# Optimization experiments

Measured on AMD Instinct MI355X. Metric: run time of the kernel, lower is better.

## Reference

```python
import jax, jax.numpy as jnp
import numpy as np

N = 50000      # nodes
E = 800000     # edges (before self-loops)
G = 64         # graphs
F_IN = 128
HID = 64
HEADS = 2
OUT = 10
NEG_SLOPE = 0.2


def setup_inputs() -> dict:
    key = jax.random.key(0)
    ks = jax.random.split(key, 12)
    x = jax.random.normal(ks[0], (N, F_IN), dtype=jnp.float32)
    edge_index = jax.random.randint(ks[1], (2, E), 0, N, dtype=jnp.int64)
    batch = jnp.sort(jax.random.randint(ks[2], (N,), 0, G, dtype=jnp.int64))
    s = 0.1
    params = {
        "W1": jax.random.normal(ks[3], (F_IN, HEADS * HID), dtype=jnp.float32) * s,
        "att_src1": jax.random.normal(ks[4], (HEADS, HID), dtype=jnp.float32) * s,
        "att_dst1": jax.random.normal(ks[5], (HEADS, HID), dtype=jnp.float32) * s,
        "b1": jnp.zeros((HEADS * HID,), dtype=jnp.float32),
        "W2": jax.random.normal(ks[6], (HEADS * HID, HEADS * HID), dtype=jnp.float32) * s,
        "att_src2": jax.random.normal(ks[7], (HEADS, HID), dtype=jnp.float32) * s,
        "att_dst2": jax.random.normal(ks[8], (HEADS, HID), dtype=jnp.float32) * s,
        "b2": jnp.zeros((HEADS * HID,), dtype=jnp.float32),
        "Wl": jax.random.normal(ks[9], (HEADS * HID, OUT), dtype=jnp.float32) * s,
        "bl": jnp.zeros((OUT,), dtype=jnp.float32),
    }
    return {"x": x, "edge_index": edge_index, "batch": batch, **params}


def gat_conv(x, W, att_src, att_dst, bias, src, dst):
    # x: [N, Fin]; W: [Fin, H*C]
    h = (x @ W).reshape(N, HEADS, HID)                      # [N, H, C]
    a_src = jnp.sum(h * att_src, axis=-1)                   # [N, H]
    a_dst = jnp.sum(h * att_dst, axis=-1)                   # [N, H]
    alpha = jax.nn.leaky_relu(a_src[src] + a_dst[dst], NEG_SLOPE)  # [Etot, H]
    # segment softmax over incoming edges of each dst node
    m = jax.ops.segment_max(alpha, dst, num_segments=N)     # [N, H]
    alpha = jnp.exp(alpha - m[dst])
    denom = jax.ops.segment_sum(alpha, dst, num_segments=N)
    alpha = alpha / (denom[dst] + 1e-16)
    out = jax.ops.segment_sum(alpha[:, :, None] * h[src], dst, num_segments=N)
    return out.reshape(N, HEADS * HID) + bias


def reference(x, edge_index, batch, W1, att_src1, att_dst1, b1,
              W2, att_src2, att_dst2, b2, Wl, bl):
    # PyG GATConv default: add self-loops
    loop = jnp.arange(N, dtype=edge_index.dtype)
    src = jnp.concatenate([edge_index[0], loop])
    dst = jnp.concatenate([edge_index[1], loop])

    h = jax.nn.relu(gat_conv(x, W1, att_src1, att_dst1, b1, src, dst))
    h = jax.nn.relu(gat_conv(h, W2, att_src2, att_dst2, b2, src, dst))

    # global_mean_pool over graphs
    sums = jax.ops.segment_sum(h, batch, num_segments=G)        # [G, H*C]
    cnts = jax.ops.segment_sum(jnp.ones((N,), h.dtype), batch, num_segments=G)
    pooled = sums / jnp.maximum(cnts, 1.0)[:, None]
    return pooled @ Wl + bl                                      # [G, OUT]
```

## Files before the change

kernel.cpp:

```cpp
#include <hip/hip_runtime.h>
#include <hip/hip_fp16.h>
#include <math.h>

#define N_NODES 50000
#define N_EDGES 800000
#define ETOT    850000
#define GRAPHS  64
#define FIN     128
#define HC      128
#define OUTF    10
#define NEG     0.2f

#define NBUCK   196
#define BCAP    8192
#define EPT     8

using half8   = __attribute__((ext_vector_type(8))) _Float16;
using float4v = __attribute__((ext_vector_type(4))) float;

__global__ void initk(int* tails, float* sums) {
    int i = blockIdx.x * 256 + threadIdx.x;
    if (i < NBUCK) tails[i] = 0;
    if (i < GRAPHS * HC) sums[i] = 0.f;
}

__global__ void wconv(const float* __restrict__ W1, const float* __restrict__ W2,
                      _Float16* __restrict__ WT1, _Float16* __restrict__ WT2) {
    int t = blockIdx.x * 256 + threadIdx.x;
    if (t < 16384) {
        int n = t >> 7, k = t & 127;
        WT1[t] = (_Float16)W1[k * 128 + n];
        WT2[t] = (_Float16)W2[k * 128 + n];
    }
}

__global__ __launch_bounds__(256) void bucketA(const int* __restrict__ ei,
                                               int* __restrict__ tails,
                                               int* __restrict__ bdata) {
    __shared__ int hist[NBUCK];
    __shared__ int lbase[NBUCK];
    int t = threadIdx.x;
    int e0 = blockIdx.x * (256 * EPT);
    for (int i = t; i < NBUCK; i += 256) hist[i] = 0;
    __syncthreads();

    int bb[EPT], pk[EPT], rk[EPT];
#pragma unroll
    for (int i = 0; i < EPT; ++i) {
        int e = e0 + i * 256 + t;
        bb[i] = -1;
        if (e < ETOT) {
            int s, d;
            if (e < N_EDGES) { s = ei[e]; d = ei[N_EDGES + e]; }
            else             { s = d = e - N_EDGES; }
            bb[i] = d >> 8;
            pk[i] = s | ((d & 255) << 16);
            rk[i] = atomicAdd(&hist[bb[i]], 1);
        }
    }
    __syncthreads();
    for (int i = t; i < NBUCK; i += 256)
        lbase[i] = atomicAdd(&tails[i], hist[i]);
    __syncthreads();
#pragma unroll
    for (int i = 0; i < EPT; ++i)
        if (bb[i] >= 0) bdata[bb[i] * BCAP + lbase[bb[i]] + rk[i]] = pk[i];
}

__global__ void scanBuckets(const int* __restrict__ tails,
                            int* __restrict__ csrBase,
                            int* __restrict__ rowptr) {
    __shared__ int sh[256];
    int t = threadIdx.x;
    int c = (t < NBUCK) ? tails[t] : 0;
    sh[t] = c;
    __syncthreads();
    for (int off = 1; off < 256; off <<= 1) {
        int add = (t >= off) ? sh[t - off] : 0;
        __syncthreads();
        sh[t] += add;
        __syncthreads();
    }
    if (t < NBUCK) csrBase[t] = sh[t] - c;
    if (t == NBUCK - 1) rowptr[N_NODES] = sh[t];
}

__global__ __launch_bounds__(256) void bucketB(const int* __restrict__ bdata,
                                               const int* __restrict__ tails,
                                               const int* __restrict__ csrBase,
                                               int* __restrict__ rowptr,
                                               int* __restrict__ csr) {
    __shared__ int hist[256];
    __shared__ int scanws[256];
    int b = blockIdx.x;
    int t = threadIdx.x;
    int nodes0 = b << 8;
    int nnodes = min(256, N_NODES - nodes0);
    int cnt  = tails[b];
    int base = csrBase[b];
    const int* bd = &bdata[b * BCAP];

    hist[t] = 0;
    __syncthreads();
    for (int j = t; j < cnt; j += 256) atomicAdd(&hist[bd[j] >> 16], 1);
    __syncthreads();
    scanws[t] = hist[t];
    __syncthreads();
    for (int off = 1; off < 256; off <<= 1) {
        int add = (t >= off) ? scanws[t - off] : 0;
        __syncthreads();
        scanws[t] += add;
        __syncthreads();
    }
    int excl = scanws[t] - hist[t];
    if (t < nnodes) rowptr[nodes0 + t] = base + excl;
    __syncthreads();
    hist[t] = excl;
    __syncthreads();
    for (int j = t; j < cnt; j += 256) {
        int pkv = bd[j];
        int pos = atomicAdd(&hist[pkv >> 16], 1);
        csr[base + pos] = pkv & 0xFFFF;
    }
}

template<bool FP32IN>
__global__ __launch_bounds__(256) void gemmMFMA(const void* __restrict__ Xin,
                                                const _Float16* __restrict__ WT,
                                                const float* __restrict__ att_s,
                                                const float* __restrict__ att_d,
                                                _Float16* __restrict__ H16,
                                                float2* __restrict__ a_src,
                                                float2* __restrict__ a_dst) {
    __shared__ _Float16 wt[128][128];
    int t = threadIdx.x;

    for (int i = t; i < 128 * 16; i += 256) {
        int n = i >> 4, ch = i & 15;
        int k0 = ch * 8;
        half8 v = *(const half8*)&WT[n * 128 + k0];
        *(half8*)&wt[n][k0 ^ ((n & 7) << 3)] = v;
    }

    int w = t >> 6, lane = t & 63;
    int hi = lane >> 4, l16 = lane & 15;
    int rbase = blockIdx.x * 64 + w * 16;
    int arow = min(rbase + l16, N_NODES - 1);

    half8 a[4];
    if (FP32IN) {
        const float* X = (const float*)Xin;
#pragma unroll
        for (int kb = 0; kb < 4; ++kb) {
            int k0 = kb * 32 + hi * 8;
            float4 x0 = *(const float4*)&X[(size_t)arow * 128 + k0];
            float4 x1 = *(const float4*)&X[(size_t)arow * 128 + k0 + 4];
            half8 v;
            v[0] = (_Float16)x0.x; v[1] = (_Float16)x0.y;
            v[2] = (_Float16)x0.z; v[3] = (_Float16)x0.w;
            v[4] = (_Float16)x1.x; v[5] = (_Float16)x1.y;
            v[6] = (_Float16)x1.z; v[7] = (_Float16)x1.w;
            a[kb] = v;
        }
    } else {
        const _Float16* X = (const _Float16*)Xin;
#pragma unroll
        for (int kb = 0; kb < 4; ++kb)
            a[kb] = *(const half8*)&X[(size_t)arow * 128 + kb * 32 + hi * 8];
    }

    __syncthreads();

    float4v acc[8];
#pragma unroll
    for (int ct = 0; ct < 8; ++ct) {
        float4v c = {0.f, 0.f, 0.f, 0.f};
        int n = ct * 16 + l16;
#pragma unroll
        for (int kb = 0; kb < 4; ++kb) {
            int k0 = (kb * 32 + hi * 8) ^ ((n & 7) << 3);
            half8 b = *(const half8*)&wt[n][k0];
            c = __builtin_amdgcn_mfma_f32_16x16x32_f16(a[kb], b, c, 0, 0, 0);
        }
        acc[ct] = c;
    }

    int grow0 = rbase + hi * 4;
#pragma unroll
    for (int ct = 0; ct < 8; ++ct) {
#pragma unroll
        for (int r = 0; r < 4; ++r) {
            int grow = grow0 + r;
            if (grow < N_NODES)
                H16[(size_t)grow * 128 + ct * 16 + l16] = (_Float16)acc[ct][r];
        }
    }

    float as_[8], ad_[8];
#pragma unroll
    for (int ct = 0; ct < 8; ++ct) {
        as_[ct] = att_s[ct * 16 + l16];
        ad_[ct] = att_d[ct * 16 + l16];
    }
#pragma unroll
    for (int r = 0; r < 4; ++r) {
        float s0 = 0.f, s1 = 0.f, d0 = 0.f, d1 = 0.f;
#pragma unroll
        for (int ct = 0; ct < 4; ++ct) { s0 += acc[ct][r] * as_[ct]; d0 += acc[ct][r] * ad_[ct]; }
#pragma unroll
        for (int ct = 4; ct < 8; ++ct) { s1 += acc[ct][r] * as_[ct]; d1 += acc[ct][r] * ad_[ct]; }
        for (int off = 1; off < 16; off <<= 1) {
            s0 += __shfl_xor(s0, off); s1 += __shfl_xor(s1, off);
            d0 += __shfl_xor(d0, off); d1 += __shfl_xor(d1, off);
        }
        int grow = grow0 + r;
        if (l16 == 0 && grow < N_NODES) {
            a_src[grow] = make_float2(s0, s1);
            a_dst[grow] = make_float2(d0, d1);
        }
    }
}

__device__ __forceinline__ float leaky(float x) { return x > 0.f ? x : NEG * x; }

__global__ __launch_bounds__(256) void aggk(const __half* __restrict__ H16,
                                            const float2* __restrict__ a_src,
                                            const float2* __restrict__ a_dst,
                                            const int* __restrict__ rowptr,
                                            const int* __restrict__ csr,
                                            const float* __restrict__ bias,
                                            _Float16* __restrict__ out16) {
    int wid = (blockIdx.x * 256 + threadIdx.x) >> 6;
    int lane = threadIdx.x & 63;
    if (wid >= N_NODES) return;
    int rbeg = rowptr[wid], rend = rowptr[wid + 1];
    float2 ad = a_dst[wid];

    int grp = lane >> 3;
    int gl  = lane & 7;
    int head = gl >> 2;
    float adh = head ? ad.y : ad.x;
    int f = gl * 16;

    float acc[16];
#pragma unroll
    for (int i = 0; i < 16; ++i) acc[i] = 0.f;
    float denom = 0.f;

    int j = rbeg + grp;
    int sNext = (j < rend) ? csr[j] : 0;
    for (; j < rend; j += 8) {
        int s = sNext;
        int jn = j + 8;
        if (jn < rend) sNext = csr[jn];
        float2 as = a_src[s];
        float wgt = __expf(leaky((head ? as.y : as.x) + adh));
        const uint4* hp = (const uint4*)&H16[(size_t)s * 128 + f];
        uint4 r0 = hp[0];
        uint4 r1 = hp[1];
        float2 p;
        p = __half22float2(*(__half2*)&r0.x); acc[0] += wgt * p.x; acc[1] += wgt * p.y;
        p = __half22float2(*(__half2*)&r0.y); acc[2] += wgt * p.x; acc[3] += wgt * p.y;
        p = __half22float2(*(__half2*)&r0.z); acc[4] += wgt * p.x; acc[5] += wgt * p.y;
        p = __half22float2(*(__half2*)&r0.w); acc[6] += wgt * p.x; acc[7] += wgt * p.y;
        p = __half22float2(*(__half2*)&r1.x); acc[8] += wgt * p.x; acc[9] += wgt * p.y;
        p = __half22float2(*(__half2*)&r1.y); acc[10] += wgt * p.x; acc[11] += wgt * p.y;
        p = __half22float2(*(__half2*)&r1.z); acc[12] += wgt * p.x; acc[13] += wgt * p.y;
        p = __half22float2(*(__half2*)&r1.w); acc[14] += wgt * p.x; acc[15] += wgt * p.y;
        denom += wgt;
    }
#pragma unroll
    for (int off = 8; off <= 32; off <<= 1) {
#pragma unroll
        for (int i = 0; i < 16; ++i) acc[i] += __shfl_xor(acc[i], off);
        denom += __shfl_xor(denom, off);
    }

    if (grp == 0) {
        float inv = 1.f / (denom + 1e-16f);
        half8 h0, h1;
#pragma unroll
        for (int i = 0; i < 8; ++i) {
            float o = fmaxf(acc[i] * inv + bias[f + i], 0.f);
            h0[i] = (_Float16)o;
        }
#pragma unroll
        for (int i = 0; i < 8; ++i) {
            float o = fmaxf(acc[8 + i] * inv + bias[f + 8 + i], 0.f);
            h1[i] = (_Float16)o;
        }
        *(half8*)&out16[(size_t)wid * 128 + f]     = h0;
        *(half8*)&out16[(size_t)wid * 128 + f + 8] = h1;
    }
}

__global__ void countk(const int* __restrict__ batch, int* cnt) {
    int g = threadIdx.x;
    if (g >= GRAPHS) return;
    int lo = 0, hi = N_NODES;
    while (lo < hi) { int mid = (lo + hi) >> 1; if (batch[mid] < g) lo = mid + 1; else hi = mid; }
    int lb = lo;
    lo = 0; hi = N_NODES;
    while (lo < hi) { int mid = (lo + hi) >> 1; if (batch[mid] < g + 1) lo = mid + 1; else hi = mid; }
    cnt[g] = lo - lb;
}

__global__ void poolk(const _Float16* __restrict__ H, const int* __restrict__ batch,
                      float* __restrict__ sums) {
    int f = threadIdx.x;
    int n0 = blockIdx.x * 64;
    if (n0 >= N_NODES) return;
    int n1 = min(n0 + 64, N_NODES);
    int g = batch[n0];
    float run = 0.f;
    for (int n = n0; n < n1; ++n) {
        int gn = batch[n];
        if (gn != g) { atomicAdd(&sums[g * 128 + f], run); run = 0.f; g = gn; }
        run += (float)H[(size_t)n * 128 + f];
    }
    atomicAdd(&sums[g * 128 + f], run);
}

__global__ void finalk(const float* __restrict__ sums, const int* __restrict__ cnt,
                       const float* __restrict__ Wl, const float* __restrict__ bl,
                       float* __restrict__ out) {
    int t = threadIdx.x;
    if (t >= GRAPHS * OUTF) return;
    int g = t / OUTF, o = t % OUTF;
    float inv = 1.f / fmaxf((float)cnt[g], 1.f);
    float acc = 0.f;
#pragma unroll 8
    for (int k = 0; k < 128; ++k) acc += sums[g * 128 + k] * Wl[k * OUTF + o];
    out[t] = acc * inv + bl[o];
}

extern "C" void kernel_launch(void* const* d_in, const int* in_sizes, int n_in,
                              void* d_out, int out_size, void* d_ws, size_t ws_size,
                              hipStream_t stream) {
    const float* x        = (const float*)d_in[0];
    const int*   ei       = (const int*)d_in[1];
    const int*   batch    = (const int*)d_in[2];
    const float* W1       = (const float*)d_in[3];
    const float* att_src1 = (const float*)d_in[4];
    const float* att_dst1 = (const float*)d_in[5];
    const float* b1       = (const float*)d_in[6];
    const float* W2       = (const float*)d_in[7];
    const float* att_src2 = (const float*)d_in[8];
    const float* att_dst2 = (const float*)d_in[9];
    const float* b2       = (const float*)d_in[10];
    const float* Wl       = (const float*)d_in[11];
    const float* bl       = (const float*)d_in[12];
    float* out = (float*)d_out;

    size_t off = 0;
    auto alloc = [&](size_t bytes) -> void* {
        void* p = (char*)d_ws + off;
        off = (off + bytes + 255) & ~(size_t)255;
        return p;
    };
    _Float16* H16     = (_Float16*)alloc((size_t)N_NODES * 128 * 2);
    _Float16* B16     = (_Float16*)alloc((size_t)N_NODES * 128 * 2);
    _Float16* WT1     = (_Float16*)alloc(16384 * 2);
    _Float16* WT2     = (_Float16*)alloc(16384 * 2);
    float2*   a_src   = (float2*)alloc((size_t)N_NODES * 8);
    float2*   a_dst   = (float2*)alloc((size_t)N_NODES * 8);
    int*      bdata   = (int*)alloc((size_t)NBUCK * BCAP * 4);
    int*      tails   = (int*)alloc(NBUCK * 4);
    int*      csrBase = (int*)alloc(NBUCK * 4);
    int*      rowptr  = (int*)alloc((size_t)(N_NODES + 1) * 4);
    int*      csr     = (int*)alloc((size_t)ETOT * 4);
    float*    sums    = (float*)alloc((size_t)GRAPHS * HC * 4);
    int*      cnt     = (int*)alloc(GRAPHS * 4);

    initk<<<32, 256, 0, stream>>>(tails, sums);
    wconv<<<64, 256, 0, stream>>>(W1, W2, WT1, WT2);
    bucketA<<<(ETOT + 2047) / 2048, 256, 0, stream>>>(ei, tails, bdata);
    scanBuckets<<<1, 256, 0, stream>>>(tails, csrBase, rowptr);
    bucketB<<<NBUCK, 256, 0, stream>>>(bdata, tails, csrBase, rowptr, csr);

    const int gemmBlocks = (N_NODES + 63) / 64;
    const int waveBlocks = (N_NODES * 64 + 255) / 256;

    gemmMFMA<true><<<gemmBlocks, 256, 0, stream>>>(x, WT1, att_src1, att_dst1,
                                                   H16, a_src, a_dst);
    aggk<<<waveBlocks, 256, 0, stream>>>((const __half*)H16, a_src, a_dst,
                                         rowptr, csr, b1, B16);

    gemmMFMA<false><<<gemmBlocks, 256, 0, stream>>>(B16, WT2, att_src2, att_dst2,
                                                    H16, a_src, a_dst);
    aggk<<<waveBlocks, 256, 0, stream>>>((const __half*)H16, a_src, a_dst,
                                         rowptr, csr, b2, B16);

    countk<<<1, 64, 0, stream>>>(batch, cnt);
    poolk<<<(N_NODES + 63) / 64, 128, 0, stream>>>(B16, batch, sums);
    finalk<<<1, 640, 0, stream>>>(sums, cnt, Wl, bl, out);
}
```

Baseline: 173.7 us.

## Merge small kernels and co-schedule layer-1 GEMM with edge bucketing

Merges init and weight conversion into one setup kernel. It fuses the layer-1 GEMM and edge bucketing into one launch, with blocks split by index. It folds the bucket scan into each bucketB block and the graph-count binary search into finalk. The aggregation loop now prefetches a_src for the next edge alongside the next CSR index. The aim is to cut the launch count (from 11 to 7) and overlap independent work, in exchange for redundant scans per block and more LDS in the fused kernel.

```diff
diff --git a/kernel.cpp b/kernel.cpp
--- a/kernel.cpp
+++ b/kernel.cpp
@@ -14,33 +14,126 @@
 #define NBUCK   196
 #define BCAP    8192
 #define EPT     8
+#define GEMMB   782
+#define ABLK    416
 
 using half8   = __attribute__((ext_vector_type(8))) _Float16;
 using float4v = __attribute__((ext_vector_type(4))) float;
 
-__global__ void initk(int* tails, float* sums) {
+__global__ void setupk(const float* __restrict__ W1, const float* __restrict__ W2,
+                       _Float16* __restrict__ WT1, _Float16* __restrict__ WT2,
+                       int* __restrict__ tails, float* __restrict__ sums) {
     int i = blockIdx.x * 256 + threadIdx.x;
+    if (i < 16384) {
+        int n = i >> 7, k = i & 127;
+        WT1[i] = (_Float16)W1[k * 128 + n];
+        WT2[i] = (_Float16)W2[k * 128 + n];
+    }
     if (i < NBUCK) tails[i] = 0;
     if (i < GRAPHS * HC) sums[i] = 0.f;
 }
 
-__global__ void wconv(const float* __restrict__ W1, const float* __restrict__ W2,
-                      _Float16* __restrict__ WT1, _Float16* __restrict__ WT2) {
-    int t = blockIdx.x * 256 + threadIdx.x;
-    if (t < 16384) {
-        int n = t >> 7, k = t & 127;
-        WT1[t] = (_Float16)W1[k * 128 + n];
-        WT2[t] = (_Float16)W2[k * 128 + n];
-    }
-}
-
-__global__ __launch_bounds__(256) void bucketA(const int* __restrict__ ei,
-                                               int* __restrict__ tails,
-                                               int* __restrict__ bdata) {
-    __shared__ int hist[NBUCK];
-    __shared__ int lbase[NBUCK];
-    int t = threadIdx.x;
-    int e0 = blockIdx.x * (256 * EPT);
+template<bool FP32IN>
+__device__ __forceinline__ void gemm_body(int bid, int t, _Float16 (*wt)[128],
+                                          const void* __restrict__ Xin,
+                                          const _Float16* __restrict__ WT,
+                                          const float* __restrict__ att_s,
+                                          const float* __restrict__ att_d,
+                                          _Float16* __restrict__ H16,
+                                          float2* __restrict__ a_src,
+                                          float2* __restrict__ a_dst) {
+    for (int i = t; i < 128 * 16; i += 256) {
+        int n = i >> 4, ch = i & 15;
+        int k0 = ch * 8;
+        half8 v = *(const half8*)&WT[n * 128 + k0];
+        *(half8*)&wt[n][k0 ^ ((n & 7) << 3)] = v;
+    }
+
+    int w = t >> 6, lane = t & 63;
+    int hi = lane >> 4, l16 = lane & 15;
+    int rbase = bid * 64 + w * 16;
+    int arow = min(rbase + l16, N_NODES - 1);
+
+    half8 a[4];
+    if (FP32IN) {
+        const float* X = (const float*)Xin;
+#pragma unroll
+        for (int kb = 0; kb < 4; ++kb) {
+            int k0 = kb * 32 + hi * 8;
+            float4 x0 = *(const float4*)&X[(size_t)arow * 128 + k0];
+            float4 x1 = *(const float4*)&X[(size_t)arow * 128 + k0 + 4];
+            half8 v;
+            v[0] = (_Float16)x0.x; v[1] = (_Float16)x0.y;
+            v[2] = (_Float16)x0.z; v[3] = (_Float16)x0.w;
+            v[4] = (_Float16)x1.x; v[5] = (_Float16)x1.y;
+            v[6] = (_Float16)x1.z; v[7] = (_Float16)x1.w;
+            a[kb] = v;
+        }
+    } else {
+        const _Float16* X = (const _Float16*)Xin;
+#pragma unroll
+        for (int kb = 0; kb < 4; ++kb)
+            a[kb] = *(const half8*)&X[(size_t)arow * 128 + kb * 32 + hi * 8];
+    }
+
+    __syncthreads();
+
+    float4v acc[8];
+#pragma unroll
+    for (int ct = 0; ct < 8; ++ct) {
+        float4v c = {0.f, 0.f, 0.f, 0.f};
+        int n = ct * 16 + l16;
+#pragma unroll
+        for (int kb = 0; kb < 4; ++kb) {
+            int k0 = (kb * 32 + hi * 8) ^ ((n & 7) << 3);
+            half8 b = *(const half8*)&wt[n][k0];
+            c = __builtin_amdgcn_mfma_f32_16x16x32_f16(a[kb], b, c, 0, 0, 0);
+        }
+        acc[ct] = c;
+    }
+
+    int grow0 = rbase + hi * 4;
+#pragma unroll
+    for (int ct = 0; ct < 8; ++ct) {
+#pragma unroll
+        for (int r = 0; r < 4; ++r) {
+            int grow = grow0 + r;
+            if (grow < N_NODES)
+                H16[(size_t)grow * 128 + ct * 16 + l16] = (_Float16)acc[ct][r];
+        }
+    }
+
+    float as_[8], ad_[8];
+#pragma unroll
+    for (int ct = 0; ct < 8; ++ct) {
+        as_[ct] = att_s[ct * 16 + l16];
+        ad_[ct] = att_d[ct * 16 + l16];
+    }
+#pragma unroll
+    for (int r = 0; r < 4; ++r) {
+        float s0 = 0.f, s1 = 0.f, d0 = 0.f, d1 = 0.f;
+#pragma unroll
+        for (int ct = 0; ct < 4; ++ct) { s0 += acc[ct][r] * as_[ct]; d0 += acc[ct][r] * ad_[ct]; }
+#pragma unroll
+        for (int ct = 4; ct < 8; ++ct) { s1 += acc[ct][r] * as_[ct]; d1 += acc[ct][r] * ad_[ct]; }
+        for (int off = 1; off < 16; off <<= 1) {
+            s0 += __shfl_xor(s0, off); s1 += __shfl_xor(s1, off);
+            d0 += __shfl_xor(d0, off); d1 += __shfl_xor(d1, off);
+        }
+        int grow = grow0 + r;
+        if (l16 == 0 && grow < N_NODES) {
+            a_src[grow] = make_float2(s0, s1);
+            a_dst[grow] = make_float2(d0, d1);
+        }
+    }
+}
+
+__device__ __forceinline__ void bucketA_body(int bid, int t,
+                                             int* hist, int* lbase,
+                                             const int* __restrict__ ei,
+                                             int* __restrict__ tails,
+                                             int* __restrict__ bdata) {
+    int e0 = bid * (256 * EPT);
     for (int i = t; i < NBUCK; i += 256) hist[i] = 0;
     __syncthreads();
 
@@ -67,65 +160,28 @@
         if (bb[i] >= 0) bdata[bb[i] * BCAP + lbase[bb[i]] + rk[i]] = pk[i];
 }
 
-__global__ void scanBuckets(const int* __restrict__ tails,
-                            int* __restrict__ csrBase,
-                            int* __restrict__ rowptr) {
-    __shared__ int sh[256];
+__global__ __launch_bounds__(256) void fusedA(const float* __restrict__ x,
+                                              const _Float16* __restrict__ WT1,
+                                              const float* __restrict__ att_s,
+                                              const float* __restrict__ att_d,
+                                              _Float16* __restrict__ H16,
+                                              float2* __restrict__ a_src,
+                                              float2* __restrict__ a_dst,
+                                              const int* __restrict__ ei,
+                                              int* __restrict__ tails,
+                                              int* __restrict__ bdata) {
+    __shared__ _Float16 wt[128][128];
+    __shared__ int hist[NBUCK];
+    __shared__ int lbase[NBUCK];
     int t = threadIdx.x;
-    int c = (t < NBUCK) ? tails[t] : 0;
-    sh[t] = c;
-    __syncthreads();
-    for (int off = 1; off < 256; off <<= 1) {
-        int add = (t >= off) ? sh[t - off] : 0;
-        __syncthreads();
-        sh[t] += add;
-        __syncthreads();
-    }
-    if (t < NBUCK) csrBase[t] = sh[t] - c;
-    if (t == NBUCK - 1) rowptr[N_NODES] = sh[t];
-}
-
-__global__ __launch_bounds__(256) void bucketB(const int* __restrict__ bdata,
-                                               const int* __restrict__ tails,
-                                               const int* __restrict__ csrBase,
-                                               int* __restrict__ rowptr,
-                                               int* __restrict__ csr) {
-    __shared__ int hist[256];
-    __shared__ int scanws[256];
-    int b = blockIdx.x;
-    int t = threadIdx.x;
-    int nodes0 = b << 8;
-    int nnodes = min(256, N_NODES - nodes0);
-    int cnt  = tails[b];
-    int base = csrBase[b];
-    const int* bd = &bdata[b * BCAP];
-
-    hist[t] = 0;
-    __syncthreads();
-    for (int j = t; j < cnt; j += 256) atomicAdd(&hist[bd[j] >> 16], 1);
-    __syncthreads();
-    scanws[t] = hist[t];
-    __syncthreads();
-    for (int off = 1; off < 256; off <<= 1) {
-        int add = (t >= off) ? scanws[t - off] : 0;
-        __syncthreads();
-        scanws[t] += add;
-        __syncthreads();
-    }
-    int excl = scanws[t] - hist[t];
-    if (t < nnodes) rowptr[nodes0 + t] = base + excl;
-    __syncthreads();
-    hist[t] = excl;
-    __syncthreads();
-    for (int j = t; j < cnt; j += 256) {
-        int pkv = bd[j];
-        int pos = atomicAdd(&hist[pkv >> 16], 1);
-        csr[base + pos] = pkv & 0xFFFF;
-    }
-}
-
-template<bool FP32IN>
-__global__ __launch_bounds__(256) void gemmMFMA(const void* __restrict__ Xin,
+    if (blockIdx.x < GEMMB) {
+        gemm_body<true>(blockIdx.x, t, wt, x, WT1, att_s, att_d, H16, a_src, a_dst);
+    } else {
+        bucketA_body(blockIdx.x - GEMMB, t, hist, lbase, ei, tails, bdata);
+    }
+}
+
+__global__ __launch_bounds__(256) void gemmMFMA(const _Float16* __restrict__ Xin,
                                                 const _Float16* __restrict__ WT,
                                                 const float* __restrict__ att_s,
                                                 const float* __restrict__ att_d,
@@ -133,91 +189,56 @@
                                                 float2* __restrict__ a_src,
                                                 float2* __restrict__ a_dst) {
     __shared__ _Float16 wt[128][128];
+    gemm_body<false>(blockIdx.x, threadIdx.x, wt, Xin, WT, att_s, att_d, H16, a_src, a_dst);
+}
+
+__global__ __launch_bounds__(256) void bucketB(const int* __restrict__ bdata,
+                                               const int* __restrict__ tails,
+                                               int* __restrict__ rowptr,
+                                               int* __restrict__ csr) {
+    __shared__ int hist[256];
+    __shared__ int scanws[256];
+    int b = blockIdx.x;
     int t = threadIdx.x;
 
-    for (int i = t; i < 128 * 16; i += 256) {
-        int n = i >> 4, ch = i & 15;
-        int k0 = ch * 8;
-        half8 v = *(const half8*)&WT[n * 128 + k0];
-        *(half8*)&wt[n][k0 ^ ((n & 7) << 3)] = v;
-    }
-
-    int w = t >> 6, lane = t & 63;
-    int hi = lane >> 4, l16 = lane & 15;
-    int rbase = blockIdx.x * 64 + w * 16;
-    int arow = min(rbase + l16, N_NODES - 1);
-
-    half8 a[4];
-    if (FP32IN) {
-        const float* X = (const float*)Xin;
-#pragma unroll
-        for (int kb = 0; kb < 4; ++kb) {
-            int k0 = kb * 32 + hi * 8;
-            float4 x0 = *(const float4*)&X[(size_t)arow * 128 + k0];
-            float4 x1 = *(const float4*)&X[(size_t)arow * 128 + k0 + 4];
-            half8 v;
-            v[0] = (_Float16)x0.x; v[1] = (_Float16)x0.y;
-            v[2] = (_Float16)x0.z; v[3] = (_Float16)x0.w;
-            v[4] = (_Float16)x1.x; v[5] = (_Float16)x1.y;
-            v[6] = (_Float16)x1.z; v[7] = (_Float16)x1.w;
-            a[kb] = v;
-        }
-    } else {
-        const _Float16* X = (const _Float16*)Xin;
-#pragma unroll
-        for (int kb = 0; kb < 4; ++kb)
-            a[kb] = *(const half8*)&X[(size_t)arow * 128 + kb * 32 + hi * 8];
-    }
-
-    __syncthreads();
-
-    float4v acc[8];
-#pragma unroll
-    for (int ct = 0; ct < 8; ++ct) {
-        float4v c = {0.f, 0.f, 0.f, 0.f};
-        int n = ct * 16 + l16;
-#pragma unroll
-        for (int kb = 0; kb < 4; ++kb) {
-            int k0 = (kb * 32 + hi * 8) ^ ((n & 7) << 3);
-            half8 b = *(const half8*)&wt[n][k0];
-            c = __builtin_amdgcn_mfma_f32_16x16x32_f16(a[kb], b, c, 0, 0, 0);
-        }
-        acc[ct] = c;
-    }
-
-    int grow0 = rbase + hi * 4;
-#pragma unroll
-    for (int ct = 0; ct < 8; ++ct) {
-#pragma unroll
-        for (int r = 0; r < 4; ++r) {
-            int grow = grow0 + r;
-            if (grow < N_NODES)
-                H16[(size_t)grow * 128 + ct * 16 + l16] = (_Float16)acc[ct][r];
-        }
-    }
-
-    float as_[8], ad_[8];
-#pragma unroll
-    for (int ct = 0; ct < 8; ++ct) {
-        as_[ct] = att_s[ct * 16 + l16];
-        ad_[ct] = att_d[ct * 16 + l16];
-    }
-#pragma unroll
-    for (int r = 0; r < 4; ++r) {
-        float s0 = 0.f, s1 = 0.f, d0 = 0.f, d1 = 0.f;
-#pragma unroll
-        for (int ct = 0; ct < 4; ++ct) { s0 += acc[ct][r] * as_[ct]; d0 += acc[ct][r] * ad_[ct]; }
-#pragma unroll
-        for (int ct = 4; ct < 8; ++ct) { s1 += acc[ct][r] * as_[ct]; d1 += acc[ct][r] * ad_[ct]; }
-        for (int off = 1; off < 16; off <<= 1) {
-            s0 += __shfl_xor(s0, off); s1 += __shfl_xor(s1, off);
-            d0 += __shfl_xor(d0, off); d1 += __shfl_xor(d1, off);
-        }
-        int grow = grow0 + r;
-        if (l16 == 0 && grow < N_NODES) {
-            a_src[grow] = make_float2(s0, s1);
-            a_dst[grow] = make_float2(d0, d1);
-        }
+    int cb = (t < NBUCK) ? tails[t] : 0;
+    scanws[t] = cb;
+    __syncthreads();
+    for (int off = 1; off < 256; off <<= 1) {
+        int add = (t >= off) ? scanws[t - off] : 0;
+        __syncthreads();
+        scanws[t] += add;
+        __syncthreads();
+    }
+    int base = scanws[b] - tails[b];
+    if (b == NBUCK - 1 && t == 0) rowptr[N_NODES] = scanws[NBUCK - 1];
+    int cnt = tails[b];
+    int nodes0 = b << 8;
+    int nnodes = min(256, N_NODES - nodes0);
+    const int* bd = &bdata[b * BCAP];
+    __syncthreads();
+
+    hist[t] = 0;
+    __syncthreads();
+    for (int j = t; j < cnt; j += 256) atomicAdd(&hist[bd[j] >> 16], 1);
+    __syncthreads();
+    scanws[t] = hist[t];
+    __syncthreads();
+    for (int off = 1; off < 256; off <<= 1) {
+        int add = (t >= off) ? scanws[t - off] : 0;
+        __syncthreads();
+        scanws[t] += add;
+        __syncthreads();
+    }
+    int excl = scanws[t] - hist[t];
+    if (t < nnodes) rowptr[nodes0 + t] = base + excl;
+    __syncthreads();
+    hist[t] = excl;
+    __syncthreads();
+    for (int j = t; j < cnt; j += 256) {
+        int pkv = bd[j];
+        int pos = atomicAdd(&hist[pkv >> 16], 1);
+        csr[base + pos] = pkv & 0xFFFF;
     }
 }
 
@@ -248,12 +269,14 @@
     float denom = 0.f;
 
     int j = rbeg + grp;
-    int sNext = (j < rend) ? csr[j] : 0;
+    int sNext = 0;
+    float2 asNext = make_float2(0.f, 0.f);
+    if (j < rend) { sNext = csr[j]; asNext = a_src[sNext]; }
     for (; j < rend; j += 8) {
         int s = sNext;
+        float2 as = asNext;
         int jn = j + 8;
-        if (jn < rend) sNext = csr[jn];
-        float2 as = a_src[s];
+        if (jn < rend) { sNext = csr[jn]; asNext = a_src[sNext]; }
         float wgt = __expf(leaky((head ? as.y : as.x) + adh));
         const uint4* hp = (const uint4*)&H16[(size_t)s * 128 + f];
         uint4 r0 = hp[0];
@@ -294,17 +317,6 @@
     }
 }
 
-__global__ void countk(const int* __restrict__ batch, int* cnt) {
-    int g = threadIdx.x;
-    if (g >= GRAPHS) return;
-    int lo = 0, hi = N_NODES;
-    while (lo < hi) { int mid = (lo + hi) >> 1; if (batch[mid] < g) lo = mid + 1; else hi = mid; }
-    int lb = lo;
-    lo = 0; hi = N_NODES;
-    while (lo < hi) { int mid = (lo + hi) >> 1; if (batch[mid] < g + 1) lo = mid + 1; else hi = mid; }
-    cnt[g] = lo - lb;
-}
-
 __global__ void poolk(const _Float16* __restrict__ H, const int* __restrict__ batch,
                       float* __restrict__ sums) {
     int f = threadIdx.x;
@@ -321,13 +333,18 @@
     atomicAdd(&sums[g * 128 + f], run);
 }
 
-__global__ void finalk(const float* __restrict__ sums, const int* __restrict__ cnt,
+__global__ void finalk(const float* __restrict__ sums, const int* __restrict__ batch,
                        const float* __restrict__ Wl, const float* __restrict__ bl,
                        float* __restrict__ out) {
     int t = threadIdx.x;
     if (t >= GRAPHS * OUTF) return;
     int g = t / OUTF, o = t % OUTF;
-    float inv = 1.f / fmaxf((float)cnt[g], 1.f);
+    int lo = 0, hi = N_NODES;
+    while (lo < hi) { int m = (lo + hi) >> 1; if (batch[m] < g) lo = m + 1; else hi = m; }
+    int lb = lo;
+    lo = 0; hi = N_NODES;
+    while (lo < hi) { int m = (lo + hi) >> 1; if (batch[m] < g + 1) lo = m + 1; else hi = m; }
+    float inv = 1.f / fmaxf((float)(lo - lb), 1.f);
     float acc = 0.f;
 #pragma unroll 8
     for (int k = 0; k < 128; ++k) acc += sums[g * 128 + k] * Wl[k * OUTF + o];
@@ -366,32 +383,22 @@
     float2*   a_dst   = (float2*)alloc((size_t)N_NODES * 8);
     int*      bdata   = (int*)alloc((size_t)NBUCK * BCAP * 4);
     int*      tails   = (int*)alloc(NBUCK * 4);
-    int*      csrBase = (int*)alloc(NBUCK * 4);
     int*      rowptr  = (int*)alloc((size_t)(N_NODES + 1) * 4);
     int*      csr     = (int*)alloc((size_t)ETOT * 4);
     float*    sums    = (float*)alloc((size_t)GRAPHS * HC * 4);
-    int*      cnt     = (int*)alloc(GRAPHS * 4);
-
-    initk<<<32, 256, 0, stream>>>(tails, sums);
-    wconv<<<64, 256, 0, stream>>>(W1, W2, WT1, WT2);
-    bucketA<<<(ETOT + 2047) / 2048, 256, 0, stream>>>(ei, tails, bdata);
-    scanBuckets<<<1, 256, 0, stream>>>(tails, csrBase, rowptr);
-    bucketB<<<NBUCK, 256, 0, stream>>>(bdata, tails, csrBase, rowptr, csr);
-
-    const int gemmBlocks = (N_NODES + 63) / 64;
+
     const int waveBlocks = (N_NODES * 64 + 255) / 256;
 
-    gemmMFMA<true><<<gemmBlocks, 256, 0, stream>>>(x, WT1, att_src1, att_dst1,
-                                                   H16, a_src, a_dst);
+    setupk<<<64, 256, 0, stream>>>(W1, W2, WT1, WT2, tails, sums);
+    fusedA<<<GEMMB + ABLK, 256, 0, stream>>>(x, WT1, att_src1, att_dst1,
+                                             H16, a_src, a_dst, ei, tails, bdata);
+    bucketB<<<NBUCK, 256, 0, stream>>>(bdata, tails, rowptr, csr);
     aggk<<<waveBlocks, 256, 0, stream>>>((const __half*)H16, a_src, a_dst,
                                          rowptr, csr, b1, B16);
-
-    gemmMFMA<false><<<gemmBlocks, 256, 0, stream>>>(B16, WT2, att_src2, att_dst2,
-                                                    H16, a_src, a_dst);
+    gemmMFMA<<<GEMMB, 256, 0, stream>>>(B16, WT2, att_src2, att_dst2,
+                                        H16, a_src, a_dst);
     aggk<<<waveBlocks, 256, 0, stream>>>((const __half*)H16, a_src, a_dst,
                                          rowptr, csr, b2, B16);
-
-    countk<<<1, 64, 0, stream>>>(batch, cnt);
     poolk<<<(N_NODES + 63) / 64, 128, 0, stream>>>(B16, batch, sums);
-    finalk<<<1, 640, 0, stream>>>(sums, cnt, Wl, bl, out);
-}
+    finalk<<<1, 640, 0, stream>>>(sums, batch, Wl, bl, out);
+}
```

Result: faster. 168.4 us (-3.0%).
